# Performance work log

Hardware: AMD Instinct MI355X
Metric: run time of the kernel (lower is better)

The kernel has to match this reference:

```python
import jax, jax.numpy as jnp
import numpy as np

N_NODES, N_EDGES, NNZ, F_IN, HID, K = 50000, 10000, 800000, 128, 512, 10


def setup_inputs() -> dict:
    key = jax.random.key(0)
    ks = jax.random.split(key, 6)
    x = jax.random.normal(ks[0], (N_NODES, F_IN), dtype=jnp.float32)
    node_idx = jax.random.randint(ks[1], (NNZ,), 0, N_NODES)
    edge_idx = jax.random.randint(ks[2], (NNZ,), 0, N_EDGES)
    hyperedge_index = jnp.stack([node_idx, edge_idx]).astype(jnp.int64)
    edge_weight = jax.random.uniform(ks[3], (N_EDGES,), dtype=jnp.float32, minval=0.5, maxval=1.5)
    theta = jax.random.normal(ks[4], (K + 1,), dtype=jnp.float32) * 0.1
    lin1_w = jax.random.normal(ks[5], (HID, F_IN), dtype=jnp.float32) * (1.0 / np.sqrt(F_IN))
    lin1_b = jnp.zeros((HID,), dtype=jnp.float32)
    return {"x": x, "hyperedge_index": hyperedge_index, "edge_weight": edge_weight,
            "theta": theta, "lin1_w": lin1_w, "lin1_b": lin1_b}


def _hyper_prop_factory(node_idx, edge_idx, edge_weight, n_nodes, n_edges):
    """Returns A_norm @ x where A_norm = Dv^-1/2 H W De^-1 H^T Dv^-1/2."""
    ones = jnp.ones_like(node_idx, dtype=edge_weight.dtype)
    d_e = jax.ops.segment_sum(ones, edge_idx, num_segments=n_edges)            # edge degree
    d_v = jax.ops.segment_sum(edge_weight[edge_idx], node_idx, num_segments=n_nodes)
    dv_is = jnp.where(d_v > 0, jax.lax.rsqrt(jnp.maximum(d_v, 1e-12)), 0.0)
    de_w = edge_weight * jnp.where(d_e > 0, 1.0 / jnp.maximum(d_e, 1e-12), 0.0)

    def prop(x):
        xv = x * dv_is[:, None]                                               # [N, F]
        m_e = jax.ops.segment_sum(xv[node_idx], edge_idx, num_segments=n_edges)
        m_e = m_e * de_w[:, None]                                             # [E, F]
        out = jax.ops.segment_sum(m_e[edge_idx], node_idx, num_segments=n_nodes)
        return out * dv_is[:, None]

    return prop


def cheb_hypergraph(x, node_idx, edge_idx, edge_weight, theta, n_nodes, n_edges):
    # L_tilde = L - I = -A_norm (lambda_max = 2). Chebyshev recurrence on L_tilde.
    prop = _hyper_prop_factory(node_idx, edge_idx, edge_weight, n_nodes, n_edges)
    t_prev = x                       # T_0
    out = theta[0] * t_prev
    t_cur = -prop(x)                 # T_1 = L_tilde x
    out = out + theta[1] * t_cur
    for k in range(2, theta.shape[0]):
        t_next = -2.0 * prop(t_cur) - t_prev   # T_k = 2 L_tilde T_{k-1} - T_{k-2}
        out = out + theta[k] * t_next
        t_prev, t_cur = t_cur, t_next
    return out


def reference(x, hyperedge_index, edge_weight, theta, lin1_w, lin1_b):
    node_idx = hyperedge_index[0]
    edge_idx = hyperedge_index[1]
    n_nodes = x.shape[0]
    n_edges = edge_weight.shape[0]
    # eval mode: both dropouts are identity
    h = cheb_hypergraph(x, node_idx, edge_idx, edge_weight, theta, n_nodes, n_edges)
    h = jnp.einsum('nf,hf->nh', h, lin1_w) + lin1_b
    # is_bns=False -> no batch norm; act_fn='relu'
    return jax.nn.relu(h)
```

## Files before the change

### kernel.cpp

```cpp
#include <hip/hip_runtime.h>


#define N_NODES 50000
#define N_EDGES 10000
#define NNZ     800000
#define F_IN    128
#define HID     512
#define F4      (F_IN / 4)
#define R16     16

typedef __attribute__((ext_vector_type(8))) short bf16x8;
typedef __attribute__((ext_vector_type(4))) float f32x4;

static __device__ __forceinline__ unsigned short f2bf(float f) {
    union { float f; unsigned u; } c; c.f = f;
    unsigned u = c.u;
    unsigned r = (u + 0x7fffu + ((u >> 16) & 1u)) >> 16;
    return (unsigned short)r;
}
static __device__ __forceinline__ float blo(unsigned u) {
    union { unsigned u; float f; } c; c.u = u << 16; return c.f;
}
static __device__ __forceinline__ float bhi(unsigned u) {
    union { unsigned u; float f; } c; c.u = u & 0xffff0000u; return c.f;
}
static __device__ __forceinline__ unsigned pack2(float lo, float hi) {
    return (unsigned)f2bf(lo) | ((unsigned)f2bf(hi) << 16);
}

__global__ void k_zero2(int* __restrict__ d_e_cnt16, int* __restrict__ n_cnt16) {
    int i = blockIdx.x * blockDim.x + threadIdx.x;
    if (i < N_NODES * 16) n_cnt16[i] = 0;
    if (i < N_EDGES * 16) d_e_cnt16[i] = 0;
}

__global__ void k_degrees(const int* __restrict__ hidx,
                          int* __restrict__ d_e_cnt16,
                          int* __restrict__ n_cnt16,
                          int* __restrict__ rank_e,
                          int* __restrict__ rank_v) {
    int i = blockIdx.x * blockDim.x + threadIdx.x;
    if (i >= NNZ) return;
    int v = hidx[i];
    int e = hidx[NNZ + i];
    v = min(max(v, 0), N_NODES - 1);
    e = min(max(e, 0), N_EDGES - 1);
    rank_e[i] = atomicAdd(&d_e_cnt16[e << 4], 1);
    rank_v[i] = atomicAdd(&n_cnt16[v << 4], 1);
}

__global__ __launch_bounds__(1024) void k_scan_blk(const int* __restrict__ counts, int n,
                                                   int stride,
                                                   int* __restrict__ out,
                                                   int* __restrict__ partial) {
    __shared__ int sd[1024];
    int tid = (int)threadIdx.x;
    int i = blockIdx.x * 1024 + tid;
    int v = (i < n) ? counts[(size_t)i * stride] : 0;
    sd[tid] = v;
    __syncthreads();
    for (int off = 1; off < 1024; off <<= 1) {
        int t = (tid >= off) ? sd[tid - off] : 0;
        __syncthreads();
        sd[tid] += t;
        __syncthreads();
    }
    if (i < n) out[i] = sd[tid] - v;
    if (tid == 1023) partial[blockIdx.x] = sd[1023];
}

__global__ void k_scan_top(int* __restrict__ partial, int nb, int* __restrict__ total_out) {
    int lane = (int)threadIdx.x;
    int v = (lane < nb) ? partial[lane] : 0;
    int incl = v;
    for (int off = 1; off < 64; off <<= 1) {
        int t = __shfl_up(incl, off);
        if (lane >= off) incl += t;
    }
    if (lane < nb) partial[lane] = incl - v;
    if (lane == 63) *total_out = incl;
}

__global__ __launch_bounds__(1024) void k_scan_add(int* __restrict__ out, int n,
                                                   const int* __restrict__ partial) {
    int i = blockIdx.x * 1024 + (int)threadIdx.x;
    if (i < n) out[i] += partial[blockIdx.x];
}

__global__ void k_fill(const int* __restrict__ hidx,
                       const int* __restrict__ edge_ptr,
                       const int* __restrict__ node_ptr,
                       const int* __restrict__ rank_e,
                       const int* __restrict__ rank_v,
                       int* __restrict__ edge_node,
                       int* __restrict__ node_edge) {
    int i = blockIdx.x * blockDim.x + threadIdx.x;
    if (i >= NNZ) return;
    int v = hidx[i];
    int e = hidx[NNZ + i];
    v = min(max(v, 0), N_NODES - 1);
    e = min(max(e, 0), N_EDGES - 1);
    edge_node[edge_ptr[e] + rank_e[i]] = v;
    node_edge[node_ptr[v] + rank_v[i]] = e;
}

__global__ void k_norms2(const float* __restrict__ ew,
                         const int* __restrict__ edge_ptr,
                         const int* __restrict__ node_ptr,
                         const int* __restrict__ node_edge,
                         float* __restrict__ dv_is,
                         float* __restrict__ de_w) {
    int i = blockIdx.x * blockDim.x + threadIdx.x;
    if (i < N_NODES) {
        int s = node_ptr[i], t = node_ptr[i + 1];
        float d = 0.f;
        for (int j = s; j < t; ++j) d += ew[node_edge[j]];
        dv_is[i] = (d > 0.f) ? rsqrtf(fmaxf(d, 1e-12f)) : 0.f;
    }
    if (i < N_EDGES) {
        int c = edge_ptr[i + 1] - edge_ptr[i];
        de_w[i] = ew[i] * ((c > 0) ? (1.f / (float)c) : 0.f);
    }
}

__global__ void k_init(const float* __restrict__ x,
                       const float* __restrict__ theta,
                       uint4* __restrict__ bufA,
                       float* __restrict__ acc) {
    int i = blockIdx.x * blockDim.x + threadIdx.x;
    if (i >= N_NODES * R16) return;
    float4 x0 = ((const float4*)x)[2 * i];
    float4 x1 = ((const float4*)x)[2 * i + 1];
    uint4 q;
    q.x = pack2(x0.x, x0.y); q.y = pack2(x0.z, x0.w);
    q.z = pack2(x1.x, x1.y); q.w = pack2(x1.z, x1.w);
    bufA[i] = q;
    float t0 = theta[0];
    float4 a0, a1;
    a0.x = t0 * x0.x; a0.y = t0 * x0.y; a0.z = t0 * x0.z; a0.w = t0 * x0.w;
    a1.x = t0 * x1.x; a1.y = t0 * x1.y; a1.z = t0 * x1.z; a1.w = t0 * x1.w;
    ((float4*)acc)[2 * i]     = a0;
    ((float4*)acc)[2 * i + 1] = a1;
}

__global__ void k_phaseA(const uint4* __restrict__ tin,
                         const float* __restrict__ dv_is,
                         const float* __restrict__ de_w,
                         const int* __restrict__ edge_ptr,
                         const int* __restrict__ edge_node,
                         uint4* __restrict__ m_e) {
    int g      = threadIdx.x >> 5;
    int stream = (threadIdx.x >> 4) & 1;
    int lane   = threadIdx.x & 15;
    int e = blockIdx.x * 8 + g;
    int s = edge_ptr[e], t = edge_ptr[e + 1];
    float a0=0.f,a1=0.f,a2=0.f,a3=0.f,a4=0.f,a5=0.f,a6=0.f,a7=0.f;
    int j = s + stream;
    for (; j + 2 < t; j += 4) {
        int v0 = edge_node[j];
        int v1 = edge_node[j + 2];
        float w0 = dv_is[v0];
        float w1 = dv_is[v1];
        uint4 q0 = tin[v0 * R16 + lane];
        uint4 q1 = tin[v1 * R16 + lane];
        a0 += w0 * blo(q0.x); a1 += w0 * bhi(q0.x);
        a2 += w0 * blo(q0.y); a3 += w0 * bhi(q0.y);
        a4 += w0 * blo(q0.z); a5 += w0 * bhi(q0.z);
        a6 += w0 * blo(q0.w); a7 += w0 * bhi(q0.w);
        a0 += w1 * blo(q1.x); a1 += w1 * bhi(q1.x);
        a2 += w1 * blo(q1.y); a3 += w1 * bhi(q1.y);
        a4 += w1 * blo(q1.z); a5 += w1 * bhi(q1.z);
        a6 += w1 * blo(q1.w); a7 += w1 * bhi(q1.w);
    }
    if (j < t) {
        int v0 = edge_node[j];
        float w0 = dv_is[v0];
        uint4 q0 = tin[v0 * R16 + lane];
        a0 += w0 * blo(q0.x); a1 += w0 * bhi(q0.x);
        a2 += w0 * blo(q0.y); a3 += w0 * bhi(q0.y);
        a4 += w0 * blo(q0.z); a5 += w0 * bhi(q0.z);
        a6 += w0 * blo(q0.w); a7 += w0 * bhi(q0.w);
    }
    a0 += __shfl_xor(a0, 16); a1 += __shfl_xor(a1, 16);
    a2 += __shfl_xor(a2, 16); a3 += __shfl_xor(a3, 16);
    a4 += __shfl_xor(a4, 16); a5 += __shfl_xor(a5, 16);
    a6 += __shfl_xor(a6, 16); a7 += __shfl_xor(a7, 16);
    if (stream == 0) {
        float w = de_w[e];
        uint4 o;
        o.x = pack2(a0 * w, a1 * w); o.y = pack2(a2 * w, a3 * w);
        o.z = pack2(a4 * w, a5 * w); o.w = pack2(a6 * w, a7 * w);
        m_e[e * R16 + lane] = o;
    }
}

__global__ void k_phaseB(const uint4* __restrict__ m_e,
                         const float* __restrict__ dv_is,
                         const int* __restrict__ node_ptr,
                         const int* __restrict__ node_edge,
                         uint4* __restrict__ tio,
                         float* __restrict__ acc,
                         const float* __restrict__ theta, int k,
                         float ca, float cb) {
    int g      = threadIdx.x >> 5;
    int stream = (threadIdx.x >> 4) & 1;
    int lane   = threadIdx.x & 15;
    int v = blockIdx.x * 8 + g;
    int s = node_ptr[v], t = node_ptr[v + 1];
    float s0=0.f,s1=0.f,s2=0.f,s3=0.f,s4=0.f,s5=0.f,s6=0.f,s7=0.f;
    int j = s + stream;
    for (; j + 2 < t; j += 4) {
        int e0 = node_edge[j];
        int e1 = node_edge[j + 2];
        uint4 q0 = m_e[e0 * R16 + lane];
        uint4 q1 = m_e[e1 * R16 + lane];
        s0 += blo(q0.x) + blo(q1.x); s1 += bhi(q0.x) + bhi(q1.x);
        s2 += blo(q0.y) + blo(q1.y); s3 += bhi(q0.y) + bhi(q1.y);
        s4 += blo(q0.z) + blo(q1.z); s5 += bhi(q0.z) + bhi(q1.z);
        s6 += blo(q0.w) + blo(q1.w); s7 += bhi(q0.w) + bhi(q1.w);
    }
    if (j < t) {
        int e0 = node_edge[j];
        uint4 q0 = m_e[e0 * R16 + lane];
        s0 += blo(q0.x); s1 += bhi(q0.x);
        s2 += blo(q0.y); s3 += bhi(q0.y);
        s4 += blo(q0.z); s5 += bhi(q0.z);
        s6 += blo(q0.w); s7 += bhi(q0.w);
    }
    s0 += __shfl_xor(s0, 16); s1 += __shfl_xor(s1, 16);
    s2 += __shfl_xor(s2, 16); s3 += __shfl_xor(s3, 16);
    s4 += __shfl_xor(s4, 16); s5 += __shfl_xor(s5, 16);
    s6 += __shfl_xor(s6, 16); s7 += __shfl_xor(s7, 16);
    if (stream == 0) {
        float sc = dv_is[v] * ca;
        float th = theta[k];
        int idx = v * R16 + lane;
        uint4 tp = tio[idx];
        float t0 = sc * s0 + cb * blo(tp.x);
        float t1 = sc * s1 + cb * bhi(tp.x);
        float t2 = sc * s2 + cb * blo(tp.y);
        float t3 = sc * s3 + cb * bhi(tp.y);
        float t4 = sc * s4 + cb * blo(tp.z);
        float t5 = sc * s5 + cb * bhi(tp.z);
        float t6 = sc * s6 + cb * blo(tp.w);
        float t7 = sc * s7 + cb * bhi(tp.w);
        uint4 tn;
        tn.x = pack2(t0, t1); tn.y = pack2(t2, t3);
        tn.z = pack2(t4, t5); tn.w = pack2(t6, t7);
        tio[idx] = tn;
        float4* acc4 = (float4*)acc;
        int ai = v * 32 + lane * 2;
        float4 a = acc4[ai];
        a.x += th * t0; a.y += th * t1; a.z += th * t2; a.w += th * t3;
        acc4[ai] = a;
        float4 b = acc4[ai + 1];
        b.x += th * t4; b.y += th * t5; b.z += th * t6; b.w += th * t7;
        acc4[ai + 1] = b;
    }
}

#define M_TILES 782
__global__ __launch_bounds__(256) void k_gemm(const float* __restrict__ A,
                                              const float* __restrict__ W,
                                              const float* __restrict__ bias,
                                              float* __restrict__ out) {
    __shared__ short Asm[64 * 136];
    __shared__ short Wsm[64 * 136];
    int id  = (int)blockIdx.x;
    int xcd = id & 7;
    int sub = id >> 3;
    int h_t = sub & 7;
    int m_i = sub >> 3;
    int m_t = xcd * 98 + m_i;
    if (m_t >= M_TILES) return;
    int m0 = m_t * 64;
    int h0 = h_t * 64;
    int tid = (int)threadIdx.x;

    const float4* A4 = (const float4*)A;
    const float4* W4 = (const float4*)W;
#pragma unroll
    for (int i = 0; i < 4; ++i) {
        int c   = tid + i * 256;
        int row = c >> 4;
        int q4  = c & 15;
        int gr = m0 + row;
        float4 a0, a1;
        if (gr < N_NODES) {
            a0 = A4[(size_t)gr * 32 + q4 * 2];
            a1 = A4[(size_t)gr * 32 + q4 * 2 + 1];
        } else {
            a0 = make_float4(0.f, 0.f, 0.f, 0.f);
            a1 = a0;
        }
        uint4 pa;
        pa.x = pack2(a0.x, a0.y); pa.y = pack2(a0.z, a0.w);
        pa.z = pack2(a1.x, a1.y); pa.w = pack2(a1.z, a1.w);
        *(uint4*)&Asm[row * 136 + q4 * 8] = pa;
        float4 w0 = W4[(size_t)(h0 + row) * 32 + q4 * 2];
        float4 w1 = W4[(size_t)(h0 + row) * 32 + q4 * 2 + 1];
        uint4 pw;
        pw.x = pack2(w0.x, w0.y); pw.y = pack2(w0.z, w0.w);
        pw.z = pack2(w1.x, w1.y); pw.w = pack2(w1.z, w1.w);
        *(uint4*)&Wsm[row * 136 + q4 * 8] = pw;
    }
    __syncthreads();

    int lane = tid & 63;
    int wv   = tid >> 6;
    int l16  = lane & 15;
    int quad = lane >> 4;

    f32x4 acc[4];
#pragma unroll
    for (int n = 0; n < 4; ++n) acc[n] = (f32x4){0.f, 0.f, 0.f, 0.f};

#pragma unroll
    for (int ks = 0; ks < 4; ++ks) {
        int k0 = ks * 32;
        bf16x8 af = *(const bf16x8*)&Asm[(wv * 16 + l16) * 136 + k0 + quad * 8];
#pragma unroll
        for (int n = 0; n < 4; ++n) {
            bf16x8 bf = *(const bf16x8*)&Wsm[(n * 16 + l16) * 136 + k0 + quad * 8];
            acc[n] = __builtin_amdgcn_mfma_f32_16x16x32_bf16(af, bf, acc[n], 0, 0, 0);
        }
    }

#pragma unroll
    for (int n = 0; n < 4; ++n) {
        float bb = bias[h0 + n * 16 + l16];
#pragma unroll
        for (int r = 0; r < 4; ++r) {
            int gr = m0 + wv * 16 + quad * 4 + r;
            if (gr < N_NODES)
                out[(size_t)gr * HID + h0 + n * 16 + l16] =
                    fmaxf(acc[n][r] + bb, 0.f);
        }
    }
}

extern "C" void kernel_launch(void* const* d_in, const int* in_sizes, int n_in,
                              void* d_out, int out_size, void* d_ws, size_t ws_size,
                              hipStream_t stream) {
    const float* x     = (const float*)d_in[0];
    const int*   hidx  = (const int*)d_in[1];
    const float* ew    = (const float*)d_in[2];
    const float* theta = (const float*)d_in[3];
    const float* w1    = (const float*)d_in[4];
    const float* b1    = (const float*)d_in[5];
    float*       out   = (float*)d_out;
    int kp1 = in_sizes[3];

    char* ob = (char*)d_out;
    size_t oo = 0;
    auto oalloc = [&](size_t bytes) -> void* {
        void* p = ob + oo;
        oo = (oo + bytes + 255) & ~(size_t)255;
        return p;
    };
    uint4* bufA      = (uint4*)oalloc((size_t)N_NODES * F_IN * 2);
    uint4* bufB      = (uint4*)oalloc((size_t)N_NODES * F_IN * 2);
    uint4* m_e       = (uint4*)oalloc((size_t)N_EDGES * F_IN * 2);
    int*   edge_node = (int*)oalloc((size_t)NNZ * 4);
    int*   node_edge = (int*)oalloc((size_t)NNZ * 4);
    int*   rank_e    = (int*)oalloc((size_t)NNZ * 4);
    int*   rank_v    = (int*)oalloc((size_t)NNZ * 4);
    int*   d_e_cnt16 = (int*)oalloc((size_t)N_EDGES * 16 * 4);
    int*   n_cnt16   = (int*)oalloc((size_t)N_NODES * 16 * 4);

    char* ws = (char*)d_ws;
    size_t off = 0;
    auto alloc = [&](size_t bytes) -> void* {
        void* p = ws + off;
        off = (off + bytes + 255) & ~(size_t)255;
        return p;
    };
    float* accv     = (float*)alloc((size_t)N_NODES * F_IN * 4);
    float* dv_is    = (float*)alloc((size_t)N_NODES * 4);
    float* de_w     = (float*)alloc((size_t)N_EDGES * 4);
    int*   edge_ptr = (int*)alloc((size_t)(N_EDGES + 1) * 4);
    int*   node_ptr = (int*)alloc((size_t)(N_NODES + 1) * 4);
    int*   part_e   = (int*)alloc(64 * 4);
    int*   part_n   = (int*)alloc(64 * 4);

    const int NB_E = (N_EDGES + 1023) / 1024;
    const int NB_N = (N_NODES + 1023) / 1024;

    k_zero2<<<(N_NODES * 16 + 255) / 256, 256, 0, stream>>>(d_e_cnt16, n_cnt16);
    k_degrees<<<(NNZ + 255) / 256, 256, 0, stream>>>(hidx, d_e_cnt16, n_cnt16, rank_e, rank_v);

    k_scan_blk<<<NB_E, 1024, 0, stream>>>(d_e_cnt16, N_EDGES, 16, edge_ptr, part_e);
    k_scan_top<<<1, 64, 0, stream>>>(part_e, NB_E, edge_ptr + N_EDGES);
    k_scan_add<<<NB_E, 1024, 0, stream>>>(edge_ptr, N_EDGES, part_e);

    k_scan_blk<<<NB_N, 1024, 0, stream>>>(n_cnt16, N_NODES, 16, node_ptr, part_n);
    k_scan_top<<<1, 64, 0, stream>>>(part_n, NB_N, node_ptr + N_NODES);
    k_scan_add<<<NB_N, 1024, 0, stream>>>(node_ptr, N_NODES, part_n);

    k_fill<<<(NNZ + 255) / 256, 256, 0, stream>>>(hidx, edge_ptr, node_ptr,
                                                  rank_e, rank_v, edge_node, node_edge);
    k_norms2<<<(N_NODES + 255) / 256, 256, 0, stream>>>(ew, edge_ptr, node_ptr,
                                                        node_edge, dv_is, de_w);
    k_init<<<(N_NODES * R16 + 255) / 256, 256, 0, stream>>>(x, theta, bufA, accv);

    for (int k = 1; k < kp1; ++k) {
        const uint4* tin = (k & 1) ? bufA : bufB;
        uint4*       tio = (k & 1) ? bufB : bufA;
        float ca = (k == 1) ? -1.f : -2.f;
        float cb = (k == 1) ? 0.f : -1.f;
        k_phaseA<<<N_EDGES / 8, 256, 0, stream>>>(tin, dv_is, de_w, edge_ptr, edge_node, m_e);
        k_phaseB<<<N_NODES / 8, 256, 0, stream>>>(m_e, dv_is, node_ptr, node_edge,
                                                  tio, accv, theta, k, ca, cb);
    }

    k_gemm<<<8 * 98 * 8, 256, 0, stream>>>(accv, w1, b1, out);
}
```

Measured before the change: 828.5 us.

## Store Chebyshev terms pre-scaled by Dv^-1/2 and use per-XCD degree counters

The Chebyshev iterates are now stored scaled by dv_is, so phaseA no longer gathers dv_is per neighbour and does plain bf16 sums with a deeper unroll of four loads. PhaseB folds dv_is squared into its scale and multiplies theta by the inverse when accumulating the unscaled output. Degree counting now uses eight counter copies indexed by blockIdx mod 8 instead of padded single counters, to cut atomic contention. A per-node offset pass then turns these copies into prefix offsets used by the fill. The rescaling changes bf16 rounding behaviour, and nodes with zero degree fall back to a weight of one.

Result: faster. 796.3 us (-3.9%).

```diff
diff --git a/kernel.cpp b/kernel.cpp
--- a/kernel.cpp
+++ b/kernel.cpp
@@ -28,25 +28,55 @@
     return (unsigned)f2bf(lo) | ((unsigned)f2bf(hi) << 16);
 }
 
-__global__ void k_zero2(int* __restrict__ d_e_cnt16, int* __restrict__ n_cnt16) {
-    int i = blockIdx.x * blockDim.x + threadIdx.x;
-    if (i < N_NODES * 16) n_cnt16[i] = 0;
-    if (i < N_EDGES * 16) d_e_cnt16[i] = 0;
+__global__ void k_zero8(int* __restrict__ cnt8_e, int* __restrict__ cnt8_n) {
+    int i = blockIdx.x * blockDim.x + threadIdx.x;
+    if (i < 8 * N_NODES) cnt8_n[i] = 0;
+    if (i < 8 * N_EDGES) cnt8_e[i] = 0;
 }
 
 __global__ void k_degrees(const int* __restrict__ hidx,
-                          int* __restrict__ d_e_cnt16,
-                          int* __restrict__ n_cnt16,
+                          int* __restrict__ cnt8_e,
+                          int* __restrict__ cnt8_n,
                           int* __restrict__ rank_e,
                           int* __restrict__ rank_v) {
     int i = blockIdx.x * blockDim.x + threadIdx.x;
     if (i >= NNZ) return;
+    int xcd = (int)blockIdx.x & 7;
     int v = hidx[i];
     int e = hidx[NNZ + i];
     v = min(max(v, 0), N_NODES - 1);
     e = min(max(e, 0), N_EDGES - 1);
-    rank_e[i] = atomicAdd(&d_e_cnt16[e << 4], 1);
-    rank_v[i] = atomicAdd(&n_cnt16[v << 4], 1);
+    int re = atomicAdd(&cnt8_e[xcd * N_EDGES + e], 1);
+    int rv = atomicAdd(&cnt8_n[xcd * N_NODES + v], 1);
+    rank_e[i] = re | (xcd << 24);
+    rank_v[i] = rv | (xcd << 24);
+}
+
+__global__ void k_off8(int* __restrict__ cnt8_e,
+                       int* __restrict__ cnt8_n,
+                       int* __restrict__ counts_e,
+                       int* __restrict__ counts_n) {
+    int i = blockIdx.x * blockDim.x + threadIdx.x;
+    if (i < N_EDGES) {
+        int s = 0;
+#pragma unroll
+        for (int x = 0; x < 8; ++x) {
+            int c = cnt8_e[x * N_EDGES + i];
+            cnt8_e[x * N_EDGES + i] = s;
+            s += c;
+        }
+        counts_e[i] = s;
+    }
+    if (i < N_NODES) {
+        int s = 0;
+#pragma unroll
+        for (int x = 0; x < 8; ++x) {
+            int c = cnt8_n[x * N_NODES + i];
+            cnt8_n[x * N_NODES + i] = s;
+            s += c;
+        }
+        counts_n[i] = s;
+    }
 }
 
 __global__ __launch_bounds__(1024) void k_scan_blk(const int* __restrict__ counts, int n,
@@ -92,6 +122,8 @@
                        const int* __restrict__ node_ptr,
                        const int* __restrict__ rank_e,
                        const int* __restrict__ rank_v,
+                       const int* __restrict__ off8_e,
+                       const int* __restrict__ off8_n,
                        int* __restrict__ edge_node,
                        int* __restrict__ node_edge) {
     int i = blockIdx.x * blockDim.x + threadIdx.x;
@@ -100,8 +132,12 @@
     int e = hidx[NNZ + i];
     v = min(max(v, 0), N_NODES - 1);
     e = min(max(e, 0), N_EDGES - 1);
-    edge_node[edge_ptr[e] + rank_e[i]] = v;
-    node_edge[node_ptr[v] + rank_v[i]] = e;
+    int pe = rank_e[i];
+    int pv = rank_v[i];
+    int xe = pe >> 24, re = pe & 0xFFFFFF;
+    int xv = pv >> 24, rv = pv & 0xFFFFFF;
+    edge_node[edge_ptr[e] + off8_e[xe * N_EDGES + e] + re] = v;
+    node_edge[node_ptr[v] + off8_n[xv * N_NODES + v] + rv] = e;
 }
 
 __global__ void k_norms2(const float* __restrict__ ew,
@@ -125,15 +161,19 @@
 
 __global__ void k_init(const float* __restrict__ x,
                        const float* __restrict__ theta,
+                       const float* __restrict__ dv_is,
                        uint4* __restrict__ bufA,
                        float* __restrict__ acc) {
     int i = blockIdx.x * blockDim.x + threadIdx.x;
     if (i >= N_NODES * R16) return;
+    int v = i >> 4;
+    float dvv = dv_is[v];
+    float w = (dvv > 0.f) ? dvv : 1.f;
     float4 x0 = ((const float4*)x)[2 * i];
     float4 x1 = ((const float4*)x)[2 * i + 1];
     uint4 q;
-    q.x = pack2(x0.x, x0.y); q.y = pack2(x0.z, x0.w);
-    q.z = pack2(x1.x, x1.y); q.w = pack2(x1.z, x1.w);
+    q.x = pack2(w * x0.x, w * x0.y); q.y = pack2(w * x0.z, w * x0.w);
+    q.z = pack2(w * x1.x, w * x1.y); q.w = pack2(w * x1.z, w * x1.w);
     bufA[i] = q;
     float t0 = theta[0];
     float4 a0, a1;
@@ -144,7 +184,6 @@
 }
 
 __global__ void k_phaseA(const uint4* __restrict__ tin,
-                         const float* __restrict__ dv_is,
                          const float* __restrict__ de_w,
                          const int* __restrict__ edge_ptr,
                          const int* __restrict__ edge_node,
@@ -156,30 +195,31 @@
     int s = edge_ptr[e], t = edge_ptr[e + 1];
     float a0=0.f,a1=0.f,a2=0.f,a3=0.f,a4=0.f,a5=0.f,a6=0.f,a7=0.f;
     int j = s + stream;
-    for (; j + 2 < t; j += 4) {
+    for (; j + 6 < t; j += 8) {
         int v0 = edge_node[j];
         int v1 = edge_node[j + 2];
-        float w0 = dv_is[v0];
-        float w1 = dv_is[v1];
+        int v2 = edge_node[j + 4];
+        int v3 = edge_node[j + 6];
         uint4 q0 = tin[v0 * R16 + lane];
         uint4 q1 = tin[v1 * R16 + lane];
-        a0 += w0 * blo(q0.x); a1 += w0 * bhi(q0.x);
-        a2 += w0 * blo(q0.y); a3 += w0 * bhi(q0.y);
-        a4 += w0 * blo(q0.z); a5 += w0 * bhi(q0.z);
-        a6 += w0 * blo(q0.w); a7 += w0 * bhi(q0.w);
-        a0 += w1 * blo(q1.x); a1 += w1 * bhi(q1.x);
-        a2 += w1 * blo(q1.y); a3 += w1 * bhi(q1.y);
-        a4 += w1 * blo(q1.z); a5 += w1 * bhi(q1.z);
-        a6 += w1 * blo(q1.w); a7 += w1 * bhi(q1.w);
-    }
-    if (j < t) {
+        uint4 q2 = tin[v2 * R16 + lane];
+        uint4 q3 = tin[v3 * R16 + lane];
+        a0 += (blo(q0.x) + blo(q1.x)) + (blo(q2.x) + blo(q3.x));
+        a1 += (bhi(q0.x) + bhi(q1.x)) + (bhi(q2.x) + bhi(q3.x));
+        a2 += (blo(q0.y) + blo(q1.y)) + (blo(q2.y) + blo(q3.y));
+        a3 += (bhi(q0.y) + bhi(q1.y)) + (bhi(q2.y) + bhi(q3.y));
+        a4 += (blo(q0.z) + blo(q1.z)) + (blo(q2.z) + blo(q3.z));
+        a5 += (bhi(q0.z) + bhi(q1.z)) + (bhi(q2.z) + bhi(q3.z));
+        a6 += (blo(q0.w) + blo(q1.w)) + (blo(q2.w) + blo(q3.w));
+        a7 += (bhi(q0.w) + bhi(q1.w)) + (bhi(q2.w) + bhi(q3.w));
+    }
+    for (; j < t; j += 2) {
         int v0 = edge_node[j];
-        float w0 = dv_is[v0];
         uint4 q0 = tin[v0 * R16 + lane];
-        a0 += w0 * blo(q0.x); a1 += w0 * bhi(q0.x);
-        a2 += w0 * blo(q0.y); a3 += w0 * bhi(q0.y);
-        a4 += w0 * blo(q0.z); a5 += w0 * bhi(q0.z);
-        a6 += w0 * blo(q0.w); a7 += w0 * bhi(q0.w);
+        a0 += blo(q0.x); a1 += bhi(q0.x);
+        a2 += blo(q0.y); a3 += bhi(q0.y);
+        a4 += blo(q0.z); a5 += bhi(q0.z);
+        a6 += blo(q0.w); a7 += bhi(q0.w);
     }
     a0 += __shfl_xor(a0, 16); a1 += __shfl_xor(a1, 16);
     a2 += __shfl_xor(a2, 16); a3 += __shfl_xor(a3, 16);
@@ -232,18 +272,20 @@
     s4 += __shfl_xor(s4, 16); s5 += __shfl_xor(s5, 16);
     s6 += __shfl_xor(s6, 16); s7 += __shfl_xor(s7, 16);
     if (stream == 0) {
-        float sc = dv_is[v] * ca;
-        float th = theta[k];
+        float dvv = dv_is[v];
+        float scf = ca * dvv * dvv;
+        float iw  = (dvv > 0.f) ? (1.f / dvv) : 1.f;
+        float thinv = theta[k] * iw;
         int idx = v * R16 + lane;
         uint4 tp = tio[idx];
-        float t0 = sc * s0 + cb * blo(tp.x);
-        float t1 = sc * s1 + cb * bhi(tp.x);
-        float t2 = sc * s2 + cb * blo(tp.y);
-        float t3 = sc * s3 + cb * bhi(tp.y);
-        float t4 = sc * s4 + cb * blo(tp.z);
-        float t5 = sc * s5 + cb * bhi(tp.z);
-        float t6 = sc * s6 + cb * blo(tp.w);
-        float t7 = sc * s7 + cb * bhi(tp.w);
+        float t0 = scf * s0 + cb * blo(tp.x);
+        float t1 = scf * s1 + cb * bhi(tp.x);
+        float t2 = scf * s2 + cb * blo(tp.y);
+        float t3 = scf * s3 + cb * bhi(tp.y);
+        float t4 = scf * s4 + cb * blo(tp.z);
+        float t5 = scf * s5 + cb * bhi(tp.z);
+        float t6 = scf * s6 + cb * blo(tp.w);
+        float t7 = scf * s7 + cb * bhi(tp.w);
         uint4 tn;
         tn.x = pack2(t0, t1); tn.y = pack2(t2, t3);
         tn.z = pack2(t4, t5); tn.w = pack2(t6, t7);
@@ -251,10 +293,10 @@
         float4* acc4 = (float4*)acc;
         int ai = v * 32 + lane * 2;
         float4 a = acc4[ai];
-        a.x += th * t0; a.y += th * t1; a.z += th * t2; a.w += th * t3;
+        a.x += thinv * t0; a.y += thinv * t1; a.z += thinv * t2; a.w += thinv * t3;
         acc4[ai] = a;
         float4 b = acc4[ai + 1];
-        b.x += th * t4; b.y += th * t5; b.z += th * t6; b.w += th * t7;
+        b.x += thinv * t4; b.y += thinv * t5; b.z += thinv * t6; b.w += thinv * t7;
         acc4[ai + 1] = b;
     }
 }
@@ -365,8 +407,10 @@
     int*   node_edge = (int*)oalloc((size_t)NNZ * 4);
     int*   rank_e    = (int*)oalloc((size_t)NNZ * 4);
     int*   rank_v    = (int*)oalloc((size_t)NNZ * 4);
-    int*   d_e_cnt16 = (int*)oalloc((size_t)N_EDGES * 16 * 4);
-    int*   n_cnt16   = (int*)oalloc((size_t)N_NODES * 16 * 4);
+    int*   cnt8_e    = (int*)oalloc((size_t)8 * N_EDGES * 4);
+    int*   cnt8_n    = (int*)oalloc((size_t)8 * N_NODES * 4);
+    int*   counts_e  = (int*)oalloc((size_t)N_EDGES * 4);
+    int*   counts_n  = (int*)oalloc((size_t)N_NODES * 4);
 
     char* ws = (char*)d_ws;
     size_t off = 0;
@@ -386,29 +430,31 @@
     const int NB_E = (N_EDGES + 1023) / 1024;
     const int NB_N = (N_NODES + 1023) / 1024;
 
-    k_zero2<<<(N_NODES * 16 + 255) / 256, 256, 0, stream>>>(d_e_cnt16, n_cnt16);
-    k_degrees<<<(NNZ + 255) / 256, 256, 0, stream>>>(hidx, d_e_cnt16, n_cnt16, rank_e, rank_v);
-
-    k_scan_blk<<<NB_E, 1024, 0, stream>>>(d_e_cnt16, N_EDGES, 16, edge_ptr, part_e);
+    k_zero8<<<(8 * N_NODES + 255) / 256, 256, 0, stream>>>(cnt8_e, cnt8_n);
+    k_degrees<<<(NNZ + 255) / 256, 256, 0, stream>>>(hidx, cnt8_e, cnt8_n, rank_e, rank_v);
+    k_off8<<<(N_NODES + 255) / 256, 256, 0, stream>>>(cnt8_e, cnt8_n, counts_e, counts_n);
+
+    k_scan_blk<<<NB_E, 1024, 0, stream>>>(counts_e, N_EDGES, 1, edge_ptr, part_e);
     k_scan_top<<<1, 64, 0, stream>>>(part_e, NB_E, edge_ptr + N_EDGES);
     k_scan_add<<<NB_E, 1024, 0, stream>>>(edge_ptr, N_EDGES, part_e);
 
-    k_scan_blk<<<NB_N, 1024, 0, stream>>>(n_cnt16, N_NODES, 16, node_ptr, part_n);
+    k_scan_blk<<<NB_N, 1024, 0, stream>>>(counts_n, N_NODES, 1, node_ptr, part_n);
     k_scan_top<<<1, 64, 0, stream>>>(part_n, NB_N, node_ptr + N_NODES);
     k_scan_add<<<NB_N, 1024, 0, stream>>>(node_ptr, N_NODES, part_n);
 
     k_fill<<<(NNZ + 255) / 256, 256, 0, stream>>>(hidx, edge_ptr, node_ptr,
-                                                  rank_e, rank_v, edge_node, node_edge);
+                                                  rank_e, rank_v, cnt8_e, cnt8_n,
+                                                  edge_node, node_edge);
     k_norms2<<<(N_NODES + 255) / 256, 256, 0, stream>>>(ew, edge_ptr, node_ptr,
                                                         node_edge, dv_is, de_w);
-    k_init<<<(N_NODES * R16 + 255) / 256, 256, 0, stream>>>(x, theta, bufA, accv);
+    k_init<<<(N_NODES * R16 + 255) / 256, 256, 0, stream>>>(x, theta, dv_is, bufA, accv);
 
     for (int k = 1; k < kp1; ++k) {
         const uint4* tin = (k & 1) ? bufA : bufB;
         uint4*       tio = (k & 1) ? bufB : bufA;
         float ca = (k == 1) ? -1.f : -2.f;
         float cb = (k == 1) ? 0.f : -1.f;
-        k_phaseA<<<N_EDGES / 8, 256, 0, stream>>>(tin, dv_is, de_w, edge_ptr, edge_node, m_e);
+        k_phaseA<<<N_EDGES / 8, 256, 0, stream>>>(tin, de_w, edge_ptr, edge_node, m_e);
         k_phaseB<<<N_NODES / 8, 256, 0, stream>>>(m_e, dv_is, node_ptr, node_edge,
                                                   tio, accv, theta, k, ca, cb);
     }
```
